# Performance work log

Measured on AMD Instinct MI355X. Metric: run time of the kernel, lower is better.

## Reference

```python
import jax, jax.numpy as jnp
import numpy as np

N_SIDE = 30            # n lines per axis -> 900 primitives
GRID = 64              # grid_size
MAX_ELEMS = 32         # max_elements_per_cell
IMG = 2048             # render resolution -> 4.19M query points


def setup_inputs() -> dict:
    # Replicate the module's line-primitive initialization (one short line per n x n cell).
    rng = np.random.default_rng(42)
    n = N_SIDE
    cell_w = 1.0 / n
    ii, jj = np.meshgrid(np.arange(n), np.arange(n), indexing='ij')
    cx = (ii + 0.5) / n + (rng.random((n, n)) - 0.5) * 0.2 * cell_w
    cy = (jj + 0.5) / n + (rng.random((n, n)) - 0.5) * 0.2 * cell_w
    ang = rng.random((n, n)) * 2.0 * np.pi
    L = 0.3 * cell_w
    dx = np.cos(ang) * L
    dy = np.sin(ang) * L
    x0 = np.clip(cx - dx, 0.0, 1.0); y0 = np.clip(cy - dy, 0.0, 1.0)
    x1 = np.clip(cx + dx, 0.0, 1.0); y1 = np.clip(cy + dy, 0.0, 1.0)
    w = 0.6 / n
    # control points layout per line block: [x0, y0, x1, y1, width, 0]
    control = np.stack([x0, y0, x1, y1, np.full((n, n), w), np.zeros((n, n))], -1)
    control = control.reshape(-1, 6).astype(np.float32)
    widths = np.full((n * n,), w, np.float32)          # stroke_widths (block[7])
    colors = rng.random((n * n, 3)).astype(np.float32)  # fill_colors
    opac = np.ones((n * n,), np.float32)                # opacities
    bg = np.zeros((3,), np.float32)                     # background_color
    key = jax.random.key(0)
    x = jax.random.uniform(key, (IMG * IMG, 2), dtype=jnp.float32)
    return {
        'x': x,
        'control_points': jnp.asarray(control),
        'stroke_widths': jnp.asarray(widths),
        'fill_colors': jnp.asarray(colors),
        'opacities': jnp.asarray(opac),
        'background_color': jnp.asarray(bg),
    }


def _build_grid(control_points, stroke_widths, G, M):
    """Scatter-build: per grid cell, list of primitive indices whose (width-expanded)
    AABB overlaps the cell, plus a count (slot-0 count in the original kernel)."""
    x0, y0, x1, y1 = control_points[:, 0], control_points[:, 1], control_points[:, 2], control_points[:, 3]
    w = stroke_widths
    xmin = jnp.minimum(x0, x1) - w; xmax = jnp.maximum(x0, x1) + w
    ymin = jnp.minimum(y0, y1) - w; ymax = jnp.maximum(y0, y1) + w
    lo = jnp.arange(G, dtype=jnp.float32) / G
    hi = (jnp.arange(G, dtype=jnp.float32) + 1.0) / G
    ox = (xmin[None, :] < hi[:, None]) & (xmax[None, :] >= lo[:, None])  # [G, N]
    oy = (ymin[None, :] < hi[:, None]) & (ymax[None, :] >= lo[:, None])  # [G, N]
    mask = (ox[:, None, :] & oy[None, :, :]).reshape(G * G, -1)          # [G*G, N]
    counts = jnp.minimum(mask.sum(-1), M).astype(jnp.int32)              # [G*G]
    # stable argsort puts hit primitives first, in ascending primitive order
    entries = jnp.argsort(~mask, axis=1)[:, :M].astype(jnp.int32)        # [G*G, M]
    return entries, counts


def reference(x, control_points, stroke_widths, fill_colors, opacities, background_color):
    G, M = GRID, MAX_ELEMS
    entries, counts = _build_grid(control_points, stroke_widths, G, M)
    ix = jnp.clip((x[:, 0] * G).astype(jnp.int32), 0, G - 1)
    iy = jnp.clip((x[:, 1] * G).astype(jnp.int32), 0, G - 1)
    cell = ix * G + iy              # [P]
    ccount = counts[cell]           # [P]
    p0 = control_points[:, 0:2]
    p1 = control_points[:, 2:4]
    init = jnp.broadcast_to(background_color.astype(x.dtype), (x.shape[0], 3))

    def step(color, slot):
        prim = entries[cell, slot]                              # [P] irregular gather
        a0 = p0[prim]                                           # [P,2]
        d = p1[prim] - a0
        rel = x - a0
        t = jnp.clip((rel * d).sum(-1) / jnp.maximum((d * d).sum(-1), 1e-12), 0.0, 1.0)
        dist = jnp.sqrt(((rel - t[:, None] * d) ** 2).sum(-1))  # point-to-segment distance
        inside = (dist <= stroke_widths[prim]) & (slot < ccount)
        a = opacities[prim] * inside.astype(color.dtype)        # [P]
        color = color * (1.0 - a[:, None]) + fill_colors[prim] * a[:, None]
        return color, None

    out, _ = jax.lax.scan(step, init, jnp.arange(M))
    return out
```

## Files before the change

kernel.cpp:

```cpp
#include <hip/hip_runtime.h>
#include <math.h>

#define GRIDN 64
#define MAXE 32
#define MAXPRIM 1024
#define EROW 36
#define SCAP2 15
#define SENTV 0xFFFF

#define WS_PACKED2   0u
#define WS_COLORS    32768u
#define WS_ETAB      49152u
#define WS_FLAG      638976u
#define WS_SUBTAB    655360u

#define CORE_EVAL(A, Bv)                                                         \
    float relx = __fsub_rn(px, A.x);                                             \
    float rely = __fsub_rn(py, A.y);                                             \
    float td = __fadd_rn(__fmul_rn(relx, A.z), __fmul_rn(rely, A.w));            \
    double inv = __hiloint2double(__float_as_int(Bv.z), __float_as_int(Bv.y));   \
    float tt = (float)((double)td * inv);                                        \
    tt = fminf(fmaxf(tt, 0.0f), 1.0f);                                           \
    float qx = __fsub_rn(relx, __fmul_rn(tt, A.z));                              \
    float qy = __fsub_rn(rely, __fmul_rn(tt, A.w));                              \
    float s2 = __fadd_rn(__fmul_rn(qx, qx), __fmul_rn(qy, qy));

__global__ __launch_bounds__(1024) void prep(const float* __restrict__ cp,
                                             const float* __restrict__ sw,
                                             const float* __restrict__ fc,
                                             const float* __restrict__ op,
                                             float4* __restrict__ packed2,
                                             float4* __restrict__ colors,
                                             int* __restrict__ etab,
                                             int* __restrict__ flagp, int nprim) {
    __shared__ float4 saabb[MAXPRIM];
    __shared__ int sbad;
    int tid = threadIdx.x;
    if (tid == 0) sbad = 0;
    for (int p = tid; p < nprim; p += 1024) {
        float x0 = cp[p * 6 + 0], y0 = cp[p * 6 + 1];
        float x1 = cp[p * 6 + 2], y1 = cp[p * 6 + 3];
        float w = sw[p];
        saabb[p] = make_float4(__fsub_rn(fminf(x0, x1), w), __fadd_rn(fmaxf(x0, x1), w),
                               __fsub_rn(fminf(y0, y1), w), __fadd_rn(fmaxf(y0, y1), w));
    }
    __syncthreads();

    int wid = tid >> 6, lane = tid & 63;
    int cell = blockIdx.x * 16 + wid;
    int ixc = cell >> 6, iyc = cell & 63;
    float lox = (float)ixc * (1.0f / GRIDN);
    float hix = (float)(ixc + 1) * (1.0f / GRIDN);
    float loy = (float)iyc * (1.0f / GRIDN);
    float hiy = (float)(iyc + 1) * (1.0f / GRIDN);
    int total = 0;
    int* row = etab + (size_t)cell * EROW;
    for (int base = 0; base < nprim; base += 64) {
        int p = base + lane;
        bool ov = false;
        if (p < nprim) {
            float4 bb = saabb[p];
            ov = (bb.x < hix) && (bb.y >= lox) && (bb.z < hiy) && (bb.w >= loy);
        }
        unsigned long long m = __ballot(ov);
        if (ov) {
            int pos = total + (int)__popcll(m & ((1ull << lane) - 1ull));
            if (pos < MAXE) row[1 + pos] = p;
        }
        total += (int)__popcll(m);
    }
    if (lane == 0) row[0] = total < MAXE ? total : MAXE;

    if (blockIdx.x == 0) {
        bool bad = false;
        for (int p = tid; p < nprim; p += 1024) {
            float x0 = cp[p * 6 + 0], y0 = cp[p * 6 + 1];
            float x1 = cp[p * 6 + 2], y1 = cp[p * 6 + 3];
            float w = sw[p];
            float dx = __fsub_rn(x1, x0);
            float dy = __fsub_rn(y1, y0);
            float dd = __fadd_rn(__fmul_rn(dx, dx), __fmul_rn(dy, dy));
            float denom = fmaxf(dd, 1e-12f);
            double inv = 1.0 / (double)denom;
            unsigned wb = __float_as_uint(w);
            bool even = (wb & 1u) == 0u;
            float wn = __uint_as_float(wb + 1u);
            double md = 0.5 * ((double)w + (double)wn);
            double m2 = md * md;
            float Tf = (float)m2;
            if ((double)Tf > m2) Tf = __uint_as_float(__float_as_uint(Tf) - 1u);
            if (!even && (double)Tf == m2) Tf = __uint_as_float(__float_as_uint(Tf) - 1u);
            unsigned long long ib = __double_as_longlong(inv);
            packed2[p * 2 + 0] = make_float4(x0, y0, dx, dy);
            packed2[p * 2 + 1] = make_float4(Tf,
                                             __uint_as_float((unsigned)(ib & 0xffffffffull)),
                                             __uint_as_float((unsigned)(ib >> 32)),
                                             w);
            float opv = op[p];
            colors[p] = make_float4(fc[p * 3 + 0], fc[p * 3 + 1], fc[p * 3 + 2], opv);
            if (opv != 1.0f) bad = true;
        }
        if (bad) atomicOr(&sbad, 1);
        __syncthreads();
        if (tid == 0) flagp[0] = sbad;
    }
}

__global__ __launch_bounds__(1024) void build_sub(const float4* __restrict__ packed2,
                                                  const int* __restrict__ etab,
                                                  unsigned short* __restrict__ subtab) {
    int t = blockIdx.x * 1024 + threadIdx.x;
    int parent = t >> 4;
    int sub = t & 15;
    int ix = parent >> 6, iy = parent & 63;
    int gx = ix * 4 + (sub >> 2), gy = iy * 4 + (sub & 3);
    double clx = (double)gx * (1.0 / 256.0);
    double chx = (double)(gx + 1) * (1.0 / 256.0);
    double cly = (double)gy * (1.0 / 256.0);
    double chy = (double)(gy + 1) * (1.0 / 256.0);
    const int* row = etab + (size_t)parent * EROW;
    int cnt = row[0];
    unsigned short* srow = subtab + (size_t)(gx * 256 + gy) * 16;
    int oc = 0;
    for (int s = 0; s < cnt; ++s) {
        int e = row[1 + s];
        float4 A = packed2[e * 2 + 0];
        float4 B = packed2[e * 2 + 1];
        double W = (double)B.w + 1e-5;
        double lx = clx - W, hx = chx + W, ly = cly - W, hy = chy + W;
        double ax = (double)A.x, ay = (double)A.y;
        double dx = (double)A.z, dy = (double)A.w;
        double t0 = 0.0, t1 = 1.0;
        bool ok = true;
        if (fabs(dx) > 1e-300) {
            double ta = (lx - ax) / dx, tb = (hx - ax) / dx;
            t0 = fmax(t0, fmin(ta, tb));
            t1 = fmin(t1, fmax(ta, tb));
        } else if (ax < lx || ax > hx) ok = false;
        if (ok) {
            if (fabs(dy) > 1e-300) {
                double ta = (ly - ay) / dy, tb = (hy - ay) / dy;
                t0 = fmax(t0, fmin(ta, tb));
                t1 = fmin(t1, fmax(ta, tb));
            } else if (ay < ly || ay > hy) ok = false;
        }
        if (ok && t0 <= t1) {
            if (oc < SCAP2) srow[1 + oc] = (unsigned short)e;
            ++oc;
        }
    }
    int filled = oc < SCAP2 ? oc : SCAP2;
    for (int k = filled; k < SCAP2; ++k) srow[1 + k] = 0;
    srow[0] = (oc <= SCAP2) ? (unsigned short)oc : (unsigned short)SENTV;
}

__device__ __forceinline__ void test_seq(int e, float px, float py, bool fast,
                                         int& win, float& cr, float& cg, float& cb,
                                         const float4* sA, const float4* sBsk,
                                         const float4* __restrict__ colors) {
    float4 A = sA[e];
    float4 Bv = sBsk[e + 4];
    CORE_EVAL(A, Bv);
    if (fast) {
        if (s2 <= Bv.x) win = e;
    } else {
        float4 C = colors[e];
        float a = (s2 <= Bv.x) ? C.w : 0.0f;
        float om = __fsub_rn(1.0f, a);
        cr = __fadd_rn(__fmul_rn(cr, om), __fmul_rn(C.x, a));
        cg = __fadd_rn(__fmul_rn(cg, om), __fmul_rn(C.y, a));
        cb = __fadd_rn(__fmul_rn(cb, om), __fmul_rn(C.z, a));
    }
}

__global__ __launch_bounds__(512) void render_ilp(const float4* __restrict__ xs4,
                                                  const float4* __restrict__ packed2,
                                                  const float4* __restrict__ colors,
                                                  const int* __restrict__ etab,
                                                  const int* __restrict__ subtab,
                                                  const float* __restrict__ bg,
                                                  const int* __restrict__ flagp,
                                                  float* __restrict__ out,
                                                  int n, int nprim) {
    __shared__ float4 sA[MAXPRIM];
    __shared__ float4 sBsk[MAXPRIM + 4];

    int tid = threadIdx.x;
    long long g0 = (long long)blockIdx.x * 1024 + (long long)tid * 2;
    bool v0 = g0 < (long long)n, v1 = (g0 + 1) < (long long)n;

    float4 P = make_float4(0.f, 0.f, 0.f, 0.f);
    if (v1) {
        P = xs4[g0 >> 1];
    } else if (v0) {
        float2 t2 = ((const float2*)xs4)[g0];
        P.x = t2.x; P.y = t2.y;
    }
    float pxa[2] = {P.x, P.z};
    float pya[2] = {P.y, P.w};
    bool vs[2] = {v0, v1};
    int par[2] = {0, 0};
    int4 lo[2], hi[2];
    const int* srowp[2];
    lo[0] = lo[1] = make_int4(0, 0, 0, 0);
    hi[0] = hi[1] = make_int4(0, 0, 0, 0);
    srowp[0] = srowp[1] = subtab;

#pragma unroll
    for (int j = 0; j < 2; ++j) {
        if (vs[j]) {
            float px = pxa[j], py = pya[j];
            int ix = (int)__fmul_rn(px, (float)GRIDN);
            ix = min(max(ix, 0), GRIDN - 1);
            int iy = (int)__fmul_rn(py, (float)GRIDN);
            iy = min(max(iy, 0), GRIDN - 1);
            par[j] = ix * GRIDN + iy;
            int sx = (int)__fmul_rn(px, 256.0f) - ix * 4; sx = min(max(sx, 0), 3);
            int sy = (int)__fmul_rn(py, 256.0f) - iy * 4; sy = min(max(sy, 0), 3);
            const int* srow = subtab + (size_t)((ix * 4 + sx) * 256 + (iy * 4 + sy)) * 8;
            srowp[j] = srow;
            lo[j] = *(const int4*)srow;
            hi[j] = *(const int4*)(srow + 4);
        }
    }

    for (int t = tid; t < nprim; t += 512) {
        sA[t] = packed2[t * 2 + 0];
        sBsk[t + 4] = packed2[t * 2 + 1];
    }
    __syncthreads();

    bool fast = (flagp[0] == 0);
    float bgr = bg[0], bgg = bg[1], bgb = bg[2];
    float res[6];

#define FGRP4(basek, ea, eb, ec, ed)                                           \
    {                                                                          \
        float4 A0 = sA[ea], Q0 = sBsk[(ea) + 4];                               \
        float4 A1 = sA[eb], Q1 = sBsk[(eb) + 4];                               \
        float4 A2 = sA[ec], Q2 = sBsk[(ec) + 4];                               \
        float4 A3 = sA[ed], Q3 = sBsk[(ed) + 4];                               \
        { CORE_EVAL(A0, Q0); if (s2 <= Q0.x && (basek) + 0 < cnt) win = (ea); }\
        { CORE_EVAL(A1, Q1); if (s2 <= Q1.x && (basek) + 1 < cnt) win = (eb); }\
        { CORE_EVAL(A2, Q2); if (s2 <= Q2.x && (basek) + 2 < cnt) win = (ec); }\
        { CORE_EVAL(A3, Q3); if (s2 <= Q3.x && (basek) + 3 < cnt) win = (ed); }\
    }
#define FGRP3(basek, ea, eb, ec)                                               \
    {                                                                          \
        float4 A0 = sA[ea], Q0 = sBsk[(ea) + 4];                               \
        float4 A1 = sA[eb], Q1 = sBsk[(eb) + 4];                               \
        float4 A2 = sA[ec], Q2 = sBsk[(ec) + 4];                               \
        { CORE_EVAL(A0, Q0); if (s2 <= Q0.x && (basek) + 0 < cnt) win = (ea); }\
        { CORE_EVAL(A1, Q1); if (s2 <= Q1.x && (basek) + 1 < cnt) win = (eb); }\
        { CORE_EVAL(A2, Q2); if (s2 <= Q2.x && (basek) + 2 < cnt) win = (ec); }\
    }

#pragma unroll
    for (int j = 0; j < 2; ++j) {
        float px = pxa[j], py = pya[j];
        float cr = bgr, cg = bgg, cb = bgb;
        int win = -1;
        unsigned lx = (unsigned)lo[j].x, ly = (unsigned)lo[j].y;
        unsigned lz = (unsigned)lo[j].z, lw = (unsigned)lo[j].w;
        unsigned hxv = (unsigned)hi[j].x, hyv = (unsigned)hi[j].y;
        unsigned hzv = (unsigned)hi[j].z, hwv = (unsigned)hi[j].w;
        int cnt = vs[j] ? (int)(lx & 0xffffu) : 0;
        if (cnt != SENTV) {
            if (fast) {
                int e0 = (int)(lx >> 16), e1 = (int)(ly & 0xffffu);
                int e2 = (int)(ly >> 16), e3 = (int)(lz & 0xffffu);
                if (cnt > 0) FGRP4(0, e0, e1, e2, e3);
                if (cnt > 4) {
                    int e4 = (int)(lz >> 16), e5 = (int)(lw & 0xffffu);
                    int e6 = (int)(lw >> 16), e7 = (int)(hxv & 0xffffu);
                    FGRP4(4, e4, e5, e6, e7);
                }
                if (cnt > 8) {
                    int e8 = (int)(hxv >> 16), e9 = (int)(hyv & 0xffffu);
                    int e10 = (int)(hyv >> 16), e11 = (int)(hzv & 0xffffu);
                    FGRP4(8, e8, e9, e10, e11);
                }
                if (cnt > 12) {
                    int e12 = (int)(hzv >> 16), e13 = (int)(hwv & 0xffffu);
                    int e14 = (int)(hwv >> 16);
                    FGRP3(12, e12, e13, e14);
                }
            } else {
                const unsigned short* sr16 = (const unsigned short*)srowp[j];
                for (int s = 0; s < cnt; ++s)
                    test_seq((int)sr16[1 + s], px, py, false, win, cr, cg, cb,
                             sA, sBsk, colors);
            }
        } else {
            const int* prow = etab + (size_t)par[j] * EROW;
            int pcnt = prow[0];
            for (int s = 0; s < pcnt; ++s)
                test_seq(prow[1 + s], px, py, fast, win, cr, cg, cb,
                         sA, sBsk, colors);
        }
        if (fast && win >= 0) {
            float4 C = colors[win];
            cr = C.x; cg = C.y; cb = C.z;
        }
        res[j * 3 + 0] = cr;
        res[j * 3 + 1] = cg;
        res[j * 3 + 2] = cb;
    }
#undef FGRP4
#undef FGRP3

    float* ob = out + g0 * 3;
    if (v1) {
        *(float2*)(ob + 0) = make_float2(res[0], res[1]);
        *(float2*)(ob + 2) = make_float2(res[2], res[3]);
        *(float2*)(ob + 4) = make_float2(res[4], res[5]);
    } else if (v0) {
        ob[0] = res[0]; ob[1] = res[1]; ob[2] = res[2];
    }
}

__global__ __launch_bounds__(1024) void render_fb(const float2* __restrict__ xs,
                                                  const float4* __restrict__ packed2,
                                                  const float4* __restrict__ colors,
                                                  const int* __restrict__ etab,
                                                  const float* __restrict__ bg,
                                                  float* __restrict__ out, int n, int nprim) {
    __shared__ float4 sA[MAXPRIM];
    __shared__ float4 sBsk[MAXPRIM + 4];
    __shared__ int sflag;
    if (threadIdx.x == 0) sflag = 0;
    __syncthreads();

    int i = blockIdx.x * 1024 + threadIdx.x;
    bool valid = i < n;
    float px = 0.0f, py = 0.0f;
    int row = 0;
    int4 c0 = make_int4(0, 0, 0, 0), c1 = make_int4(0, 0, 0, 0);
    if (valid) {
        float2 pxy = xs[i];
        px = pxy.x; py = pxy.y;
        int ix = (int)__fmul_rn(px, (float)GRIDN);
        ix = min(max(ix, 0), GRIDN - 1);
        int iy = (int)__fmul_rn(py, (float)GRIDN);
        iy = min(max(iy, 0), GRIDN - 1);
        row = (ix * GRIDN + iy) * EROW;
        c0 = *(const int4*)(etab + row);
        c1 = *(const int4*)(etab + row + 4);
    }
    for (int t = threadIdx.x; t < nprim; t += 1024) {
        sA[t] = packed2[t * 2 + 0];
        sBsk[t + 4] = packed2[t * 2 + 1];
        if (colors[t].w != 1.0f) sflag = 1;
    }
    __syncthreads();
    int cnt = valid ? c0.x : 0;
    float cr = bg[0], cg = bg[1], cb = bg[2];
    int win = -1;
    bool fast = (sflag == 0);
    if (cnt > 0) test_seq(c0.y, px, py, fast, win, cr, cg, cb, sA, sBsk, colors);
    if (cnt > 1) test_seq(c0.z, px, py, fast, win, cr, cg, cb, sA, sBsk, colors);
    if (cnt > 2) test_seq(c0.w, px, py, fast, win, cr, cg, cb, sA, sBsk, colors);
    if (cnt > 3) test_seq(c1.x, px, py, fast, win, cr, cg, cb, sA, sBsk, colors);
    if (cnt > 4) test_seq(c1.y, px, py, fast, win, cr, cg, cb, sA, sBsk, colors);
    if (cnt > 5) test_seq(c1.z, px, py, fast, win, cr, cg, cb, sA, sBsk, colors);
    if (cnt > 6) test_seq(c1.w, px, py, fast, win, cr, cg, cb, sA, sBsk, colors);
    for (int base = 7; base < cnt; base += 4) {
        int4 c = *(const int4*)(etab + row + 1 + base);
        if (base + 0 < cnt) test_seq(c.x, px, py, fast, win, cr, cg, cb, sA, sBsk, colors);
        if (base + 1 < cnt) test_seq(c.y, px, py, fast, win, cr, cg, cb, sA, sBsk, colors);
        if (base + 2 < cnt) test_seq(c.z, px, py, fast, win, cr, cg, cb, sA, sBsk, colors);
        if (base + 3 < cnt) test_seq(c.w, px, py, fast, win, cr, cg, cb, sA, sBsk, colors);
    }
    if (valid) {
        if (fast && win >= 0) {
            float4 C = colors[win];
            cr = C.x; cg = C.y; cb = C.z;
        }
        out[(size_t)i * 3 + 0] = cr;
        out[(size_t)i * 3 + 1] = cg;
        out[(size_t)i * 3 + 2] = cb;
    }
}

extern "C" void kernel_launch(void* const* d_in, const int* in_sizes, int n_in,
                              void* d_out, int out_size, void* d_ws, size_t ws_size,
                              hipStream_t stream) {
    const float* x  = (const float*)d_in[0];
    const float* cp = (const float*)d_in[1];
    const float* sw = (const float*)d_in[2];
    const float* fc = (const float*)d_in[3];
    const float* op = (const float*)d_in[4];
    const float* bg = (const float*)d_in[5];
    float* out = (float*)d_out;

    int npts  = in_sizes[0] / 2;
    int nprim = in_sizes[2];

    char* ws = (char*)d_ws;
    float4* packed2 = (float4*)(ws + WS_PACKED2);
    float4* colors  = (float4*)(ws + WS_COLORS);
    int* etab       = (int*)(ws + WS_ETAB);
    int* flagp      = (int*)(ws + WS_FLAG);
    unsigned short* subtab = (unsigned short*)(ws + WS_SUBTAB);

    size_t need = (size_t)WS_SUBTAB + 65536u * 32u;
    bool use_sub = (ws_size >= need);

    prep<<<GRIDN * GRIDN / 16, 1024, 0, stream>>>(cp, sw, fc, op, packed2, colors,
                                                  etab, flagp, nprim);
    if (use_sub) {
        build_sub<<<64, 1024, 0, stream>>>(packed2, etab, subtab);
        int nblk = (npts + 1023) / 1024;
        render_ilp<<<nblk, 512, 0, stream>>>((const float4*)x, packed2, colors,
                                             etab, (const int*)subtab, bg, flagp,
                                             out, npts, nprim);
    } else {
        render_fb<<<(npts + 1023) / 1024, 1024, 0, stream>>>((const float2*)x, packed2,
                                                             colors, etab, bg, out,
                                                             npts, nprim);
    }
}
```

Baseline: 58.55 us.

## Fuse sub-grid table build into prep kernel and add sched group barriers

Folds the separate build_sub kernel into the prep kernel. Each block keeps its 16 cells' candidate lists, segment geometry and widths in shared memory, and 256 threads build the 4x4 sub-cell tables straight from LDS. This removes one kernel launch and the global round trip through etab/packed2. The change also adds sched_group_barrier hints in the fast-path group macros to interleave LDS reads with VALU work. In the fallback path prep2 now also writes into subtab, which may lie outside a workspace that is too small.

```diff
diff --git a/kernel.cpp b/kernel.cpp
--- a/kernel.cpp
+++ b/kernel.cpp
@@ -13,6 +13,8 @@
 #define WS_ETAB      49152u
 #define WS_FLAG      638976u
 #define WS_SUBTAB    655360u
+
+#define SGB __builtin_amdgcn_sched_group_barrier
 
 #define CORE_EVAL(A, Bv)                                                         \
     float relx = __fsub_rn(px, A.x);                                             \
@@ -25,16 +27,21 @@
     float qy = __fsub_rn(rely, __fmul_rn(tt, A.w));                              \
     float s2 = __fadd_rn(__fmul_rn(qx, qx), __fmul_rn(qy, qy));
 
-__global__ __launch_bounds__(1024) void prep(const float* __restrict__ cp,
-                                             const float* __restrict__ sw,
-                                             const float* __restrict__ fc,
-                                             const float* __restrict__ op,
-                                             float4* __restrict__ packed2,
-                                             float4* __restrict__ colors,
-                                             int* __restrict__ etab,
-                                             int* __restrict__ flagp, int nprim) {
+__global__ __launch_bounds__(1024) void prep2(const float* __restrict__ cp,
+                                              const float* __restrict__ sw,
+                                              const float* __restrict__ fc,
+                                              const float* __restrict__ op,
+                                              float4* __restrict__ packed2,
+                                              float4* __restrict__ colors,
+                                              int* __restrict__ etab,
+                                              int* __restrict__ flagp,
+                                              unsigned short* __restrict__ subtab,
+                                              int nprim) {
     __shared__ float4 saabb[MAXPRIM];
-    __shared__ int sbad;
+    __shared__ float4 sseg[MAXPRIM];
+    __shared__ float  sww[MAXPRIM];
+    __shared__ int    srows[16][EROW];
+    __shared__ int    sbad;
     int tid = threadIdx.x;
     if (tid == 0) sbad = 0;
     for (int p = tid; p < nprim; p += 1024) {
@@ -43,33 +50,86 @@
         float w = sw[p];
         saabb[p] = make_float4(__fsub_rn(fminf(x0, x1), w), __fadd_rn(fmaxf(x0, x1), w),
                                __fsub_rn(fminf(y0, y1), w), __fadd_rn(fmaxf(y0, y1), w));
+        sseg[p] = make_float4(x0, y0, __fsub_rn(x1, x0), __fsub_rn(y1, y0));
+        sww[p] = w;
     }
     __syncthreads();
 
     int wid = tid >> 6, lane = tid & 63;
     int cell = blockIdx.x * 16 + wid;
-    int ixc = cell >> 6, iyc = cell & 63;
-    float lox = (float)ixc * (1.0f / GRIDN);
-    float hix = (float)(ixc + 1) * (1.0f / GRIDN);
-    float loy = (float)iyc * (1.0f / GRIDN);
-    float hiy = (float)(iyc + 1) * (1.0f / GRIDN);
-    int total = 0;
-    int* row = etab + (size_t)cell * EROW;
-    for (int base = 0; base < nprim; base += 64) {
-        int p = base + lane;
-        bool ov = false;
-        if (p < nprim) {
-            float4 bb = saabb[p];
-            ov = (bb.x < hix) && (bb.y >= lox) && (bb.z < hiy) && (bb.w >= loy);
-        }
-        unsigned long long m = __ballot(ov);
-        if (ov) {
-            int pos = total + (int)__popcll(m & ((1ull << lane) - 1ull));
-            if (pos < MAXE) row[1 + pos] = p;
-        }
-        total += (int)__popcll(m);
-    }
-    if (lane == 0) row[0] = total < MAXE ? total : MAXE;
+    {
+        int ixc = cell >> 6, iyc = cell & 63;
+        float lox = (float)ixc * (1.0f / GRIDN);
+        float hix = (float)(ixc + 1) * (1.0f / GRIDN);
+        float loy = (float)iyc * (1.0f / GRIDN);
+        float hiy = (float)(iyc + 1) * (1.0f / GRIDN);
+        int total = 0;
+        int* row = etab + (size_t)cell * EROW;
+        for (int base = 0; base < nprim; base += 64) {
+            int p = base + lane;
+            bool ov = false;
+            if (p < nprim) {
+                float4 bb = saabb[p];
+                ov = (bb.x < hix) && (bb.y >= lox) && (bb.z < hiy) && (bb.w >= loy);
+            }
+            unsigned long long m = __ballot(ov);
+            if (ov) {
+                int pos = total + (int)__popcll(m & ((1ull << lane) - 1ull));
+                if (pos < MAXE) { row[1 + pos] = p; srows[wid][1 + pos] = p; }
+            }
+            total += (int)__popcll(m);
+        }
+        if (lane == 0) {
+            int c = total < MAXE ? total : MAXE;
+            row[0] = c;
+            srows[wid][0] = c;
+        }
+    }
+    __syncthreads();
+
+    if (tid < 256) {
+        int lp = tid >> 4;
+        int sub = tid & 15;
+        int pcell = blockIdx.x * 16 + lp;
+        int ix = pcell >> 6, iy = pcell & 63;
+        int gx = ix * 4 + (sub >> 2), gy = iy * 4 + (sub & 3);
+        double clx = (double)gx * (1.0 / 256.0);
+        double chx = (double)(gx + 1) * (1.0 / 256.0);
+        double cly = (double)gy * (1.0 / 256.0);
+        double chy = (double)(gy + 1) * (1.0 / 256.0);
+        int cnt = srows[lp][0];
+        unsigned short* srow = subtab + (size_t)(gx * 256 + gy) * 16;
+        int oc = 0;
+        for (int s = 0; s < cnt; ++s) {
+            int e = srows[lp][1 + s];
+            float4 A = sseg[e];
+            double W = (double)sww[e] + 1e-5;
+            double lx = clx - W, hx = chx + W, ly = cly - W, hy = chy + W;
+            double ax = (double)A.x, ay = (double)A.y;
+            double dx = (double)A.z, dy = (double)A.w;
+            double t0 = 0.0, t1 = 1.0;
+            bool ok = true;
+            if (fabs(dx) > 1e-300) {
+                double ta = (lx - ax) / dx, tb = (hx - ax) / dx;
+                t0 = fmax(t0, fmin(ta, tb));
+                t1 = fmin(t1, fmax(ta, tb));
+            } else if (ax < lx || ax > hx) ok = false;
+            if (ok) {
+                if (fabs(dy) > 1e-300) {
+                    double ta = (ly - ay) / dy, tb = (hy - ay) / dy;
+                    t0 = fmax(t0, fmin(ta, tb));
+                    t1 = fmin(t1, fmax(ta, tb));
+                } else if (ay < ly || ay > hy) ok = false;
+            }
+            if (ok && t0 <= t1) {
+                if (oc < SCAP2) srow[1 + oc] = (unsigned short)e;
+                ++oc;
+            }
+        }
+        int filled = oc < SCAP2 ? oc : SCAP2;
+        for (int k = filled; k < SCAP2; ++k) srow[1 + k] = 0;
+        srow[0] = (oc <= SCAP2) ? (unsigned short)oc : (unsigned short)SENTV;
+    }
 
     if (blockIdx.x == 0) {
         bool bad = false;
@@ -106,54 +166,6 @@
     }
 }
 
-__global__ __launch_bounds__(1024) void build_sub(const float4* __restrict__ packed2,
-                                                  const int* __restrict__ etab,
-                                                  unsigned short* __restrict__ subtab) {
-    int t = blockIdx.x * 1024 + threadIdx.x;
-    int parent = t >> 4;
-    int sub = t & 15;
-    int ix = parent >> 6, iy = parent & 63;
-    int gx = ix * 4 + (sub >> 2), gy = iy * 4 + (sub & 3);
-    double clx = (double)gx * (1.0 / 256.0);
-    double chx = (double)(gx + 1) * (1.0 / 256.0);
-    double cly = (double)gy * (1.0 / 256.0);
-    double chy = (double)(gy + 1) * (1.0 / 256.0);
-    const int* row = etab + (size_t)parent * EROW;
-    int cnt = row[0];
-    unsigned short* srow = subtab + (size_t)(gx * 256 + gy) * 16;
-    int oc = 0;
-    for (int s = 0; s < cnt; ++s) {
-        int e = row[1 + s];
-        float4 A = packed2[e * 2 + 0];
-        float4 B = packed2[e * 2 + 1];
-        double W = (double)B.w + 1e-5;
-        double lx = clx - W, hx = chx + W, ly = cly - W, hy = chy + W;
-        double ax = (double)A.x, ay = (double)A.y;
-        double dx = (double)A.z, dy = (double)A.w;
-        double t0 = 0.0, t1 = 1.0;
-        bool ok = true;
-        if (fabs(dx) > 1e-300) {
-            double ta = (lx - ax) / dx, tb = (hx - ax) / dx;
-            t0 = fmax(t0, fmin(ta, tb));
-            t1 = fmin(t1, fmax(ta, tb));
-        } else if (ax < lx || ax > hx) ok = false;
-        if (ok) {
-            if (fabs(dy) > 1e-300) {
-                double ta = (ly - ay) / dy, tb = (hy - ay) / dy;
-                t0 = fmax(t0, fmin(ta, tb));
-                t1 = fmin(t1, fmax(ta, tb));
-            } else if (ay < ly || ay > hy) ok = false;
-        }
-        if (ok && t0 <= t1) {
-            if (oc < SCAP2) srow[1 + oc] = (unsigned short)e;
-            ++oc;
-        }
-    }
-    int filled = oc < SCAP2 ? oc : SCAP2;
-    for (int k = filled; k < SCAP2; ++k) srow[1 + k] = 0;
-    srow[0] = (oc <= SCAP2) ? (unsigned short)oc : (unsigned short)SENTV;
-}
-
 __device__ __forceinline__ void test_seq(int e, float px, float py, bool fast,
                                          int& win, float& cr, float& cg, float& cb,
                                          const float4* sA, const float4* sBsk,
@@ -244,6 +256,8 @@
         { CORE_EVAL(A1, Q1); if (s2 <= Q1.x && (basek) + 1 < cnt) win = (eb); }\
         { CORE_EVAL(A2, Q2); if (s2 <= Q2.x && (basek) + 2 < cnt) win = (ec); }\
         { CORE_EVAL(A3, Q3); if (s2 <= Q3.x && (basek) + 3 < cnt) win = (ed); }\
+        SGB(0x100, 8, 0);                               \
+        SGB(0x002, 80, 0);                          \
     }
 #define FGRP3(basek, ea, eb, ec)                                               \
     {                                                                          \
@@ -253,6 +267,8 @@
         { CORE_EVAL(A0, Q0); if (s2 <= Q0.x && (basek) + 0 < cnt) win = (ea); }\
         { CORE_EVAL(A1, Q1); if (s2 <= Q1.x && (basek) + 1 < cnt) win = (eb); }\
         { CORE_EVAL(A2, Q2); if (s2 <= Q2.x && (basek) + 2 < cnt) win = (ec); }\
+        SGB(0x100, 6, 0);                                                      \
+        SGB(0x002, 60, 0);                                                     \
     }
 
 #pragma unroll
@@ -406,15 +422,16 @@
     size_t need = (size_t)WS_SUBTAB + 65536u * 32u;
     bool use_sub = (ws_size >= need);
 
-    prep<<<GRIDN * GRIDN / 16, 1024, 0, stream>>>(cp, sw, fc, op, packed2, colors,
-                                                  etab, flagp, nprim);
     if (use_sub) {
-        build_sub<<<64, 1024, 0, stream>>>(packed2, etab, subtab);
+        prep2<<<GRIDN * GRIDN / 16, 1024, 0, stream>>>(cp, sw, fc, op, packed2, colors,
+                                                       etab, flagp, subtab, nprim);
         int nblk = (npts + 1023) / 1024;
         render_ilp<<<nblk, 512, 0, stream>>>((const float4*)x, packed2, colors,
                                              etab, (const int*)subtab, bg, flagp,
                                              out, npts, nprim);
     } else {
+        prep2<<<GRIDN * GRIDN / 16, 1024, 0, stream>>>(cp, sw, fc, op, packed2, colors,
+                                                       etab, flagp, subtab, nprim);
         render_fb<<<(npts + 1023) / 1024, 1024, 0, stream>>>((const float2*)x, packed2,
                                                              colors, etab, bg, out,
                                                              npts, nprim);
```

After: 53.05 us. 9.4% less time.
